# Kernel optimization log

Hardware: AMD Instinct MI355X
Metric: run time of the kernel (lower is better)

## Reference

```python
import jax, jax.numpy as jnp
import numpy as np

WS = (8, 8)          # window_size -> S = 64
NUM_HEADS = 4
DIM = 128


def _relative_position_index(ws):
    wh, ww = ws
    coords = np.stack(np.meshgrid(np.arange(wh), np.arange(ww), indexing='ij'))  # (2,Wh,Ww)
    cf = coords.reshape(2, -1)                                   # (2, Wh*Ww)
    rel = cf[:, :, None] - cf[:, None, :]                        # (2, S, S)
    rel = rel.transpose(1, 2, 0).astype(np.int64)                # (S, S, 2)
    rel[:, :, 0] += wh - 1
    rel[:, :, 1] += ww - 1
    rel[:, :, 0] *= 2 * ww - 1
    return rel.sum(-1)                                           # (S, S)


def setup_inputs() -> dict:
    key = jax.random.key(0)
    k = jax.random.split(key, 6)
    B, S, N, C = 128, WS[0] * WS[1], 32, DIM
    num_rel = (2 * WS[0] - 1) * (2 * WS[1] - 1)
    return {
        'x': jax.random.normal(k[0], (B, S, N, C), dtype=jnp.float32),
        'qkv_w': jax.random.normal(k[1], (3 * C, C), dtype=jnp.float32) * 0.02,
        'qkv_b': jnp.zeros((3 * C,), dtype=jnp.float32),
        'proj_w': jax.random.normal(k[2], (C, C), dtype=jnp.float32) * 0.02,
        'proj_b': jnp.zeros((C,), dtype=jnp.float32),
        'bias_table': jax.random.normal(k[3], (num_rel, NUM_HEADS), dtype=jnp.float32) * 0.02,
    }


def reference(x, qkv_w, qkv_b, proj_w, proj_b, bias_table):
    B, S, N, C = x.shape
    H = NUM_HEADS
    D = N * C // H                      # effective head dim
    scale = (C // H) ** -0.5            # matches head_dim = dim // num_heads in __init__

    xf = x.reshape(B, S * N, C)
    qkv = xf @ qkv_w.T + qkv_b          # (B, S*N, 3C)
    qkv = qkv.reshape(B, S, 3, H, D).transpose(2, 0, 3, 1, 4)  # (3, B, H, S, D)
    q, k, v = qkv[0], qkv[1], qkv[2]

    rel_idx = jnp.asarray(_relative_position_index(WS))        # (S, S) int
    bias = bias_table[rel_idx.reshape(-1)].reshape(S, S, H).transpose(2, 0, 1)  # (H,S,S)

    attn = jnp.einsum('bhsd,bhtd->bhst', q, k) * scale + bias[None]
    attn = jax.nn.softmax(attn, axis=-1)

    out = jnp.einsum('bhst,bhtd->bhsd', attn, v)               # (B,H,S,D)
    out = out.transpose(0, 2, 1, 3).reshape(B, S * N, C)
    out = out @ proj_w.T + proj_b
    return out.reshape(B, S, N, C)
```

## Files before the change

kernel.cpp:

```cpp
#include <hip/hip_runtime.h>
#include <cmath>


typedef short bf16x8 __attribute__((ext_vector_type(8)));
typedef float f32x4  __attribute__((ext_vector_type(4)));
#define MFMA16 __builtin_amdgcn_mfma_f32_16x16x32_bf16

__device__ __forceinline__ unsigned rne16(float f) {
    unsigned u = __float_as_uint(f);
    return (u + 0x7fffu + ((u >> 16) & 1u)) & 0xffff0000u;
}
__device__ __forceinline__ void cvt8(float4 a, float4 b, bf16x8& H, bf16x8& L) {
    float f[8] = {a.x, a.y, a.z, a.w, b.x, b.y, b.z, b.w};
    #pragma unroll
    for (int i = 0; i < 8; ++i) {
        unsigned r = rne16(f[i]);
        H[i] = (short)(r >> 16);
        float fh = __uint_as_float(r);
        L[i] = (short)(rne16(f[i] - fh) >> 16);
    }
}
__device__ __forceinline__ void cvt8h(float4 a, float4 b, bf16x8& H) {
    float f[8] = {a.x, a.y, a.z, a.w, b.x, b.y, b.z, b.w};
    #pragma unroll
    for (int i = 0; i < 8; ++i) H[i] = (short)(rne16(f[i]) >> 16);
}

__global__ void split_w(const float* __restrict__ qw, unsigned short* __restrict__ wsp) {
    int idx = blockIdx.x * 256 + threadIdx.x;
    if (idx >= 49152) return;
    int j = idx >> 7, c = idx & 127;
    float v = qw[idx];
    unsigned r = rne16(v);
    unsigned rl = rne16(v - __uint_as_float(r));
    int dest = (((j >> 5) * 16 + (c >> 3)) * 32 + (j & 31)) * 8 + (c & 7);
    wsp[dest] = (unsigned short)(r >> 16);
    wsp[49152 + dest] = (unsigned short)(rl >> 16);
}
__global__ void split_pw(const float* __restrict__ pw, unsigned short* __restrict__ pwsp) {
    int idx = blockIdx.x * 256 + threadIdx.x;
    if (idx >= 16384) return;
    int cp = idx >> 7, c = idx & 127;
    float v = pw[idx];
    unsigned r = rne16(v);
    unsigned rl = rne16(v - __uint_as_float(r));
    int dest = ((c >> 3) * 128 + cp) * 8 + (c & 7);
    pwsp[dest] = (unsigned short)(r >> 16);
    pwsp[16384 + dest] = (unsigned short)(rl >> 16);
}

constexpr int A9_QC0 = 0,     A9_KC0 = 8320;
constexpr int A9_QC1 = 16640, A9_KC1 = 24960;
constexpr int A9_P   = 33280;
constexpr int A9_SMA = 41600;
constexpr int A9_SMB = 42112;
constexpr int A9_VC0 = 0,     A9_VC1 = 8320;
constexpr int A9_LDS = 42624;

__global__ __launch_bounds__(512, 6)
void attn_mfma9(const float* __restrict__ x,
                const float* __restrict__ qkv_b,
                const float* __restrict__ bias_table,
                const unsigned short* __restrict__ wsp,
                float* __restrict__ out)
{
    __shared__ __attribute__((aligned(128))) char lds[A9_LDS];
    const int tid = threadIdx.x;
    const int lane = tid & 63;
    const int w = tid >> 6;
    const int l15 = lane & 15, lg = lane >> 4;
    const int qt = w & 3, ch = w >> 2;
    const int rowbase = qt * 16;
    const int b = blockIdx.x >> 2, h = blockIdx.x & 3;
    const float* __restrict__ xb = x + (size_t)b * 262144;
    const float* xrow0 = xb + (size_t)(rowbase + l15) * 4096 + lg * 8;

    bf16x8 aH[4];
    bf16x8 kH[4];
    int cur_na = -1, cur_nk = -1;

    auto loadfrags = [&](int n0, bf16x8 (&H)[4]) {
        const float* p = xrow0 + (size_t)n0 * 128;
        #pragma unroll
        for (int ks = 0; ks < 4; ++ks) {
            float4 a = *(const float4*)(p + ks * 32);
            float4 c = *(const float4*)(p + ks * 32 + 4);
            cvt8h(a, c, H[ks]);
        }
    };

    auto prod32 = [&](const bf16x8 (&H)[4], int j0, f32x4 (&acc)[2]) {
        const unsigned short* wb = wsp + (size_t)(j0 >> 5) * 4096;
        #pragma unroll
        for (int ks = 0; ks < 4; ++ks) {
            #pragma unroll
            for (int ct = 0; ct < 2; ++ct) {
                int gct = ch * 2 + ct;
                int ro = (gct >> 1) * 4096 + ((ks * 4 + lg) * 32 + (gct & 1) * 16 + l15) * 8;
                bf16x8 bh = *(const bf16x8*)(wb + ro);
                acc[ct] = MFMA16(H[ks], bh, acc[ct], 0, 0, 0);
            }
        }
    };

    auto storeP32 = [&](int base, f32x4 (&acc)[2], int j0) {
        #pragma unroll
        for (int ct = 0; ct < 2; ++ct) {
            int d = (ch * 2 + ct) * 16 + l15;
            float bias = qkv_b[j0 + d];
            int dofs = (d >> 3) * 1040 + (d & 7) * 2;
            #pragma unroll
            for (int reg = 0; reg < 4; ++reg) {
                int s = rowbase + lg * 4 + reg;
                *(unsigned short*)(lds + base + dofs + s * 16) =
                    (unsigned short)(rne16(acc[ct][reg] + bias) >> 16);
            }
        }
    };

    auto prodQK = [&](int cc) {
        int remq = h * 1024 + 64 * cc;
        int nq = remq / 384, j0q = remq - nq * 384;
        int remk = 4096 + h * 1024 + 64 * cc;
        int nk = remk / 384, j0k = remk - nk * 384;
        if (nq != cur_na) { loadfrags(nq, aH); cur_na = nq; }
        if (nk != cur_nk) { loadfrags(nk, kH); cur_nk = nk; }
        f32x4 qa[2];
        #pragma unroll
        for (int i = 0; i < 2; ++i) qa[i] = (f32x4){0.f, 0.f, 0.f, 0.f};
        prod32(aH, j0q, qa);
        storeP32((cc & 1) ? A9_QC1 : A9_QC0, qa, j0q);
        f32x4 ka[2];
        #pragma unroll
        for (int i = 0; i < 2; ++i) ka[i] = (f32x4){0.f, 0.f, 0.f, 0.f};
        prod32(kH, j0k, ka);
        storeP32((cc & 1) ? A9_KC1 : A9_KC0, ka, j0k);
    };

    f32x4 accQK[2];
    #pragma unroll
    for (int tt = 0; tt < 2; ++tt) accQK[tt] = (f32x4){0.f, 0.f, 0.f, 0.f};

    prodQK(0);
    __syncthreads();

    for (int cc = 0; cc < 16; ++cc) {
        if (cc < 15) prodQK(cc + 1);

        int qcb = (cc & 1) ? A9_QC1 : A9_QC0;
        int kcb = (cc & 1) ? A9_KC1 : A9_KC0;
        #pragma unroll
        for (int kst = 0; kst < 2; ++kst) {
            int grp = (kst * 4 + lg) * 1040;
            bf16x8 qh = *(const bf16x8*)(lds + qcb + grp + (rowbase + l15) * 16);
            #pragma unroll
            for (int tt = 0; tt < 2; ++tt) {
                int trow = ((ch * 2 + tt) * 16 + l15) * 16;
                bf16x8 kh = *(const bf16x8*)(lds + kcb + grp + trow);
                accQK[tt] = MFMA16(qh, kh, accQK[tt], 0, 0, 0);
            }
        }
        __syncthreads();
    }

    {
        const float scale = 0.17677669529663687f;
        float* smA = (float*)(lds + A9_SMA);
        float* smB = (float*)(lds + A9_SMB);
        float ex[4][2];
        #pragma unroll
        for (int reg = 0; reg < 4; ++reg) {
            int s = rowbase + lg * 4 + reg;
            int i1 = s >> 3, j1 = s & 7;
            float m = -1e30f;
            #pragma unroll
            for (int tt = 0; tt < 2; ++tt) {
                int t = (ch * 2 + tt) * 16 + l15;
                int i2 = t >> 3, j2 = t & 7;
                float L = accQK[tt][reg] * scale
                        + bias_table[((i1 - i2 + 7) * 15 + (j1 - j2 + 7)) * 4 + h];
                ex[reg][tt] = L;
                m = fmaxf(m, L);
            }
            m = fmaxf(m, __shfl_xor(m, 1));
            m = fmaxf(m, __shfl_xor(m, 2));
            m = fmaxf(m, __shfl_xor(m, 4));
            m = fmaxf(m, __shfl_xor(m, 8));
            if (l15 == 0) smA[ch * 64 + s] = m;
        }
        __syncthreads();
        #pragma unroll
        for (int reg = 0; reg < 4; ++reg) {
            int s = rowbase + lg * 4 + reg;
            float mg = fmaxf(smA[s], smA[64 + s]);
            float e0 = __expf(ex[reg][0] - mg);
            float e1 = __expf(ex[reg][1] - mg);
            ex[reg][0] = e0; ex[reg][1] = e1;
            float sum = e0 + e1;
            sum += __shfl_xor(sum, 1);
            sum += __shfl_xor(sum, 2);
            sum += __shfl_xor(sum, 4);
            sum += __shfl_xor(sum, 8);
            if (l15 == 0) smB[ch * 64 + s] = sum;
        }
        __syncthreads();
        #pragma unroll
        for (int reg = 0; reg < 4; ++reg) {
            int s = rowbase + lg * 4 + reg;
            float inv = 1.f / (smB[s] + smB[64 + s]);
            #pragma unroll
            for (int tt = 0; tt < 2; ++tt) {
                int t = (ch * 2 + tt) * 16 + l15;
                int off = (t >> 3) * 1040 + s * 16 + (t & 7) * 2;
                *(unsigned short*)(lds + A9_P + off) =
                    (unsigned short)(rne16(ex[reg][tt] * inv) >> 16);
            }
        }
    }

    cur_na = -1;
    float* ob = out + (size_t)b * 262144;

    auto prodV = [&](int cc) {
        int remv = 8192 + h * 1024 + 64 * cc;
        int nv = remv / 384, j0v = remv - nv * 384;
        if (nv != cur_na) { loadfrags(nv, aH); cur_na = nv; }
        f32x4 va[2];
        #pragma unroll
        for (int i = 0; i < 2; ++i) va[i] = (f32x4){0.f, 0.f, 0.f, 0.f};
        prod32(aH, j0v, va);
        int vcb = (cc & 1) ? A9_VC1 : A9_VC0;
        #pragma unroll
        for (int ct = 0; ct < 2; ++ct) {
            int d = (ch * 2 + ct) * 16 + l15;
            float bias = qkv_b[j0v + d];
            #pragma unroll
            for (int reg = 0; reg < 4; ++reg) {
                int t = rowbase + lg * 4 + reg;
                int off = (t >> 3) * 1040 + d * 16 + (t & 7) * 2;
                *(unsigned short*)(lds + vcb + off) =
                    (unsigned short)(rne16(va[ct][reg] + bias) >> 16);
            }
        }
    };

    prodV(0);
    __syncthreads();

    for (int cc = 0; cc < 16; ++cc) {
        if (cc < 15) prodV(cc + 1);

        int vcb = (cc & 1) ? A9_VC1 : A9_VC0;
        f32x4 o[2];
        #pragma unroll
        for (int i = 0; i < 2; ++i) o[i] = (f32x4){0.f, 0.f, 0.f, 0.f};
        #pragma unroll
        for (int kst = 0; kst < 2; ++kst) {
            bf16x8 pf = *(const bf16x8*)(lds + A9_P + (kst * 4 + lg) * 1040 + (rowbase + l15) * 16);
            int vgrp = (kst * 4 + lg) * 1040;
            #pragma unroll
            for (int dt = 0; dt < 2; ++dt) {
                int drow = ((ch * 2 + dt) * 16 + l15) * 16;
                bf16x8 vh = *(const bf16x8*)(lds + vcb + vgrp + drow);
                o[dt] = MFMA16(pf, vh, o[dt], 0, 0, 0);
            }
        }

        #pragma unroll
        for (int reg = 0; reg < 4; ++reg) {
            int s = rowbase + lg * 4 + reg;
            float* orow = ob + (size_t)(s * 32 + h * 8 + (cc >> 1)) * 128 + (cc & 1) * 64;
            #pragma unroll
            for (int dt = 0; dt < 2; ++dt)
                orow[(ch * 2 + dt) * 16 + l15] = o[dt][reg];
        }
        __syncthreads();
    }
}

__global__ __launch_bounds__(256, 4)
void proj_mfma(const unsigned short* __restrict__ pwsp,
               const float* __restrict__ pb,
               float* __restrict__ io)
{
    const int tid = threadIdx.x;
    const int lane = tid & 63;
    const int w = tid >> 6;
    const int l15 = lane & 15, lg = lane >> 4;
    const size_t rbase = (size_t)blockIdx.x * 64 + w * 16;

    const float* rp = io + (rbase + l15) * 128 + lg * 8;
    bf16x8 aH[4], aL[4];
    #pragma unroll
    for (int ks = 0; ks < 4; ++ks) {
        float4 a = *(const float4*)(rp + ks * 32);
        float4 c = *(const float4*)(rp + ks * 32 + 4);
        cvt8(a, c, aH[ks], aL[ks]);
    }

    f32x4 acc[8];
    #pragma unroll
    for (int i = 0; i < 8; ++i) acc[i] = (f32x4){0.f, 0.f, 0.f, 0.f};

    #pragma unroll
    for (int ks = 0; ks < 4; ++ks) {
        #pragma unroll
        for (int ct = 0; ct < 8; ++ct) {
            int ro = ((ks * 4 + lg) * 128 + ct * 16 + l15) * 8;
            bf16x8 bh = *(const bf16x8*)(pwsp + ro);
            bf16x8 bl = *(const bf16x8*)(pwsp + 16384 + ro);
            acc[ct] = MFMA16(aH[ks], bh, acc[ct], 0, 0, 0);
            acc[ct] = MFMA16(aH[ks], bl, acc[ct], 0, 0, 0);
            acc[ct] = MFMA16(aL[ks], bh, acc[ct], 0, 0, 0);
        }
    }

    #pragma unroll
    for (int ct = 0; ct < 8; ++ct) {
        float bias = pb[ct * 16 + l15];
        #pragma unroll
        for (int reg = 0; reg < 4; ++reg)
            io[(rbase + lg * 4 + reg) * 128 + ct * 16 + l15] = acc[ct][reg] + bias;
    }
}

constexpr int QC_OFF = 0;
constexpr int KC_OFF = 8320;
constexpr int VC_OFF = 24960;
constexpr int P_OFF  = 41856;
constexpr int LDS_TOT = 50176;

__global__ __launch_bounds__(256, 2)
void attn_mfma(const float* __restrict__ x,
               const float* __restrict__ qkv_b,
               const float* __restrict__ bias_table,
               const unsigned short* __restrict__ wsp,
               float* __restrict__ out)
{
    __shared__ __attribute__((aligned(128))) char lds[LDS_TOT];
    const int tid = threadIdx.x;
    const int lane = tid & 63;
    const int w = tid >> 6;
    const int l15 = lane & 15, lg = lane >> 4;
    const int rowbase = 16 * w;
    const int b = blockIdx.x >> 2, h = blockIdx.x & 3;
    const float* __restrict__ xb = x + (size_t)b * 262144;
    const float* xrow0 = xb + ((size_t)(rowbase + l15) * 32) * 128 + lg * 8;

    bf16x8 aH[4], aL[4];
    bf16x8 kH[4], kL[4];
    int cur_na = -1, cur_nk = -1;

    auto loadfrags = [&](int n0, bf16x8 (&H)[4], bf16x8 (&L)[4]) {
        const float* p = xrow0 + (size_t)n0 * 128;
        #pragma unroll
        for (int ks = 0; ks < 4; ++ks) {
            float4 a = *(const float4*)(p + ks * 32);
            float4 c = *(const float4*)(p + ks * 32 + 4);
            cvt8(a, c, H[ks], L[ks]);
        }
    };

    auto mm_band = [&](const bf16x8 (&H)[4], const bf16x8 (&L)[4], int band,
                       f32x4& a0, f32x4& a1) {
        const unsigned short* wb = wsp + (size_t)band * 4096;
        #pragma unroll
        for (int ks = 0; ks < 4; ++ks) {
            int ro = ((ks * 4 + lg) * 32 + l15) * 8;
            bf16x8 b0h = *(const bf16x8*)(wb + ro);
            bf16x8 b0l = *(const bf16x8*)(wb + 49152 + ro);
            bf16x8 b1h = *(const bf16x8*)(wb + ro + 128);
            bf16x8 b1l = *(const bf16x8*)(wb + 49152 + ro + 128);
            a0 = MFMA16(H[ks], b0h, a0, 0, 0, 0);
            a0 = MFMA16(H[ks], b0l, a0, 0, 0, 0);
            a0 = MFMA16(L[ks], b0h, a0, 0, 0, 0);
            a1 = MFMA16(H[ks], b1h, a1, 0, 0, 0);
            a1 = MFMA16(H[ks], b1l, a1, 0, 0, 0);
            a1 = MFMA16(L[ks], b1h, a1, 0, 0, 0);
        }
    };

    auto store_rc = [&](char* base, f32x4 a0, f32x4 a1, float b0, float b1) {
        #pragma unroll
        for (int reg = 0; reg < 4; ++reg) {
            int s = rowbase + lg * 4 + reg;
            {
                float v = a0[reg] + b0;
                int i = l15;
                int off = (i >> 3) * 1040 + s * 16 + (i & 7) * 2;
                unsigned r = rne16(v);
                *(unsigned short*)(base + off) = (unsigned short)(r >> 16);
                *(unsigned short*)(base + 4160 + off) =
                    (unsigned short)(rne16(v - __uint_as_float(r)) >> 16);
            }
            {
                float v = a1[reg] + b1;
                int i = 16 + l15;
                int off = (i >> 3) * 1040 + s * 16 + (i & 7) * 2;
                unsigned r = rne16(v);
                *(unsigned short*)(base + off) = (unsigned short)(r >> 16);
                *(unsigned short*)(base + 4160 + off) =
                    (unsigned short)(rne16(v - __uint_as_float(r)) >> 16);
            }
        }
    };

    f32x4 accQK[4];
    #pragma unroll
    for (int tt = 0; tt < 4; ++tt) accQK[tt] = (f32x4){0.f, 0.f, 0.f, 0.f};

    int buf = 0;
    for (int ccc = 0; ccc < 32; ++ccc) {
        int remq = h * 1024 + 32 * ccc;
        int nq = remq / 384, j0q = remq - nq * 384, bandq = j0q >> 5;
        int remk = 4096 + h * 1024 + 32 * ccc;
        int nk = remk / 384, j0k = remk - nk * 384, bandk = j0k >> 5;
        if (nq != cur_na) { loadfrags(nq, aH, aL); cur_na = nq; }
        if (nk != cur_nk) { loadfrags(nk, kH, kL); cur_nk = nk; }

        f32x4 q0 = (f32x4){0.f,0.f,0.f,0.f}, q1 = (f32x4){0.f,0.f,0.f,0.f};
        mm_band(aH, aL, bandq, q0, q1);
        store_rc(lds + QC_OFF, q0, q1, qkv_b[j0q + l15], qkv_b[j0q + 16 + l15]);

        f32x4 k0 = (f32x4){0.f,0.f,0.f,0.f}, k1 = (f32x4){0.f,0.f,0.f,0.f};
        mm_band(kH, kL, bandk, k0, k1);
        store_rc(lds + KC_OFF + buf * 8320, k0, k1, qkv_b[j0k + l15], qkv_b[j0k + 16 + l15]);

        __syncthreads();

        const char* qc = lds + QC_OFF + lg * 1040 + (rowbase + l15) * 16;
        bf16x8 qah = *(const bf16x8*)qc;
        bf16x8 qal = *(const bf16x8*)(qc + 4160);
        #pragma unroll
        for (int tt = 0; tt < 4; ++tt) {
            const char* kc = lds + KC_OFF + buf * 8320 + lg * 1040 + (tt * 16 + l15) * 16;
            bf16x8 kbh = *(const bf16x8*)kc;
            bf16x8 kbl = *(const bf16x8*)(kc + 4160);
            accQK[tt] = MFMA16(qah, kbh, accQK[tt], 0, 0, 0);
            accQK[tt] = MFMA16(qah, kbl, accQK[tt], 0, 0, 0);
            accQK[tt] = MFMA16(qal, kbh, accQK[tt], 0, 0, 0);
        }
        buf ^= 1;
    }

    {
        const float scale = 0.17677669529663687f;
        #pragma unroll
        for (int reg = 0; reg < 4; ++reg) {
            int s = rowbase + lg * 4 + reg;
            int i1 = s >> 3, j1 = s & 7;
            float Lv[4];
            float m = -1e30f;
            #pragma unroll
            for (int tt = 0; tt < 4; ++tt) {
                int t = tt * 16 + l15;
                int i2 = t >> 3, j2 = t & 7;
                float L = accQK[tt][reg] * scale
                        + bias_table[((i1 - i2 + 7) * 15 + (j1 - j2 + 7)) * 4 + h];
                Lv[tt] = L;
                m = fmaxf(m, L);
            }
            m = fmaxf(m, __shfl_xor(m, 1));
            m = fmaxf(m, __shfl_xor(m, 2));
            m = fmaxf(m, __shfl_xor(m, 4));
            m = fmaxf(m, __shfl_xor(m, 8));
            float sum = 0.f;
            #pragma unroll
            for (int tt = 0; tt < 4; ++tt) { Lv[tt] = __expf(Lv[tt] - m); sum += Lv[tt]; }
            sum += __shfl_xor(sum, 1);
            sum += __shfl_xor(sum, 2);
            sum += __shfl_xor(sum, 4);
            sum += __shfl_xor(sum, 8);
            float inv = 1.f / sum;
            #pragma unroll
            for (int tt = 0; tt < 4; ++tt) {
                int t = tt * 16 + l15;
                int off = (t >> 3) * 1040 + s * 16 + (t & 7) * 2;
                *(unsigned short*)(lds + P_OFF + off) = (unsigned short)(rne16(Lv[tt] * inv) >> 16);
            }
        }
    }

    cur_na = -1;
    int bufv = 0;
    float* ob = out + (size_t)b * 262144;
    for (int ccc = 0; ccc < 32; ++ccc) {
        int remv = 8192 + h * 1024 + 32 * ccc;
        int nv = remv / 384, j0v = remv - nv * 384, bandv = j0v >> 5;
        if (nv != cur_na) { loadfrags(nv, aH, aL); cur_na = nv; }

        f32x4 v0 = (f32x4){0.f,0.f,0.f,0.f}, v1 = (f32x4){0.f,0.f,0.f,0.f};
        mm_band(aH, aL, bandv, v0, v1);
        {
            char* base = lds + VC_OFF + bufv * 8448;
            float b0 = qkv_b[j0v + l15], b1 = qkv_b[j0v + 16 + l15];
            #pragma unroll
            for (int reg = 0; reg < 4; ++reg) {
                int t = rowbase + lg * 4 + reg;
                {
                    float v = v0[reg] + b0;
                    int i = l15;
                    int off = (t >> 3) * 528 + i * 16 + (t & 7) * 2;
                    unsigned r = rne16(v);
                    *(unsigned short*)(base + off) = (unsigned short)(r >> 16);
                    *(unsigned short*)(base + 4224 + off) =
                        (unsigned short)(rne16(v - __uint_as_float(r)) >> 16);
                }
                {
                    float v = v1[reg] + b1;
                    int i = 16 + l15;
                    int off = (t >> 3) * 528 + i * 16 + (t & 7) * 2;
                    unsigned r = rne16(v);
                    *(unsigned short*)(base + off) = (unsigned short)(r >> 16);
                    *(unsigned short*)(base + 4224 + off) =
                        (unsigned short)(rne16(v - __uint_as_float(r)) >> 16);
                }
            }
        }
        __syncthreads();

        f32x4 o0 = (f32x4){0.f,0.f,0.f,0.f}, o1 = (f32x4){0.f,0.f,0.f,0.f};
        #pragma unroll
        for (int ks = 0; ks < 2; ++ks) {
            bf16x8 pf = *(const bf16x8*)(lds + P_OFF + (ks * 4 + lg) * 1040 + (rowbase + l15) * 16);
            const char* vb = lds + VC_OFF + bufv * 8448 + (ks * 4 + lg) * 528;
            bf16x8 v0h = *(const bf16x8*)(vb + l15 * 16);
            bf16x8 v0l = *(const bf16x8*)(vb + 4224 + l15 * 16);
            bf16x8 v1h = *(const bf16x8*)(vb + (16 + l15) * 16);
            bf16x8 v1l = *(const bf16x8*)(vb + 4224 + (16 + l15) * 16);
            o0 = MFMA16(pf, v0h, o0, 0, 0, 0);
            o0 = MFMA16(pf, v0l, o0, 0, 0, 0);
            o1 = MFMA16(pf, v1h, o1, 0, 0, 0);
            o1 = MFMA16(pf, v1l, o1, 0, 0, 0);
        }
        bufv ^= 1;

        #pragma unroll
        for (int reg = 0; reg < 4; ++reg) {
            int s = rowbase + lg * 4 + reg;
            {
                int d = 32 * ccc + l15;
                ob[(s * 32 + h * 8 + (d >> 7)) * 128 + (d & 127)] = o0[reg];
            }
            {
                int d = 32 * ccc + 16 + l15;
                ob[(s * 32 + h * 8 + (d >> 7)) * 128 + (d & 127)] = o1[reg];
            }
        }
    }
}

constexpr int LDS_B = 128 * 132 + 64 * 132;

__global__ __launch_bounds__(256, 1)
void proj_inplace(const float* __restrict__ pw,
                  const float* __restrict__ pb,
                  float* __restrict__ io)
{
    __shared__ float lds[LDS_B];
    float* pwt  = lds;
    float* rows = lds + 128 * 132;
    const int tid = threadIdx.x;

    for (int idx = tid; idx < 128 * 128; idx += 256) {
        const int c = idx >> 7, cp = idx & 127;
        pwt[cp * 132 + c] = pw[idx];
    }
    const int rb = tid >> 5;
    const int cg = tid & 31;
    const float4 pbv = *(const float4*)(pb + cg * 4);

    for (int it = 0; it < 8; ++it) {
        const size_t base = ((size_t)blockIdx.x * 8 + it) * 64;
        __syncthreads();
        for (int f = tid; f < 64 * 32; f += 256) {
            const int r = f >> 5, c4 = f & 31;
            *(float4*)(rows + r * 132 + c4 * 4) =
                *(const float4*)(io + (base + r) * 128 + c4 * 4);
        }
        __syncthreads();
        float acc[8][4] = {};
        #pragma unroll 2
        for (int cp = 0; cp < 128; ++cp) {
            const float4 wv = *(const float4*)(pwt + cp * 132 + cg * 4);
            #pragma unroll
            for (int rr = 0; rr < 8; ++rr) {
                const float xv = rows[(rb * 8 + rr) * 132 + cp];
                acc[rr][0] += xv * wv.x;
                acc[rr][1] += xv * wv.y;
                acc[rr][2] += xv * wv.z;
                acc[rr][3] += xv * wv.w;
            }
        }
        #pragma unroll
        for (int rr = 0; rr < 8; ++rr) {
            float4 o;
            o.x = acc[rr][0] + pbv.x;
            o.y = acc[rr][1] + pbv.y;
            o.z = acc[rr][2] + pbv.z;
            o.w = acc[rr][3] + pbv.w;
            *(float4*)(io + (base + rb * 8 + rr) * 128 + cg * 4) = o;
        }
    }
}

extern "C" void kernel_launch(void* const* d_in, const int* in_sizes, int n_in,
                              void* d_out, int out_size, void* d_ws, size_t ws_size,
                              hipStream_t stream)
{
    const float* x          = (const float*)d_in[0];
    const float* qkv_w      = (const float*)d_in[1];
    const float* qkv_b      = (const float*)d_in[2];
    const float* proj_w     = (const float*)d_in[3];
    const float* proj_b     = (const float*)d_in[4];
    const float* bias_table = (const float*)d_in[5];
    float* out = (float*)d_out;

    if (ws_size >= 262144 && d_ws != nullptr) {
        unsigned short* wsp = (unsigned short*)d_ws;
        unsigned short* pwsp = wsp + 98304;
        split_w<<<dim3(192), dim3(256), 0, stream>>>(qkv_w, wsp);
        split_pw<<<dim3(64), dim3(256), 0, stream>>>(proj_w, pwsp);
        attn_mfma9<<<dim3(512), dim3(512), 0, stream>>>(x, qkv_b, bias_table, wsp, out);
        proj_mfma<<<dim3(4096), dim3(256), 0, stream>>>(pwsp, proj_b, out);
    } else if (ws_size >= 196608 && d_ws != nullptr) {
        unsigned short* wsp = (unsigned short*)d_ws;
        split_w<<<dim3(192), dim3(256), 0, stream>>>(qkv_w, wsp);
        attn_mfma<<<dim3(512), dim3(256), 0, stream>>>(x, qkv_b, bias_table, wsp, out);
        proj_inplace<<<dim3(512), dim3(256), 0, stream>>>(proj_w, proj_b, out);
    }
}
```

Before: 220.4 us.

## Split attention blocks by query half to double grid size

The fused attention kernel now launches 1024 blocks instead of 512, each handling 32 of the 64 query rows for one batch/head. Wave roles are remapped so Q projection, QK scores, softmax and PV each use one MFMA tile per wave, with smaller Q/P LDS buffers. This raises parallelism and lowers LDS use per block. In exchange, each block still computes the full K and V projections, so that work is duplicated across the two query halves and total reads of x and FLOPs rise.

```diff
diff --git a/kernel.cpp b/kernel.cpp
--- a/kernel.cpp
+++ b/kernel.cpp
@@ -49,70 +49,114 @@
     pwsp[16384 + dest] = (unsigned short)(rl >> 16);
 }
 
-constexpr int A9_QC0 = 0,     A9_KC0 = 8320;
-constexpr int A9_QC1 = 16640, A9_KC1 = 24960;
-constexpr int A9_P   = 33280;
-constexpr int A9_SMA = 41600;
-constexpr int A9_SMB = 42112;
-constexpr int A9_VC0 = 0,     A9_VC1 = 8320;
-constexpr int A9_LDS = 42624;
+constexpr int A12_QC0 = 0,     A12_KC0 = 4224;
+constexpr int A12_QC1 = 12544, A12_KC1 = 16768;
+constexpr int A12_P   = 25088;
+constexpr int A12_SMA = 29312;
+constexpr int A12_SMB = 29824;
+constexpr int A12_VC0 = 0,     A12_VC1 = 12544;
+constexpr int A12_LDS = 30336;
 
 __global__ __launch_bounds__(512, 6)
-void attn_mfma9(const float* __restrict__ x,
-                const float* __restrict__ qkv_b,
-                const float* __restrict__ bias_table,
-                const unsigned short* __restrict__ wsp,
-                float* __restrict__ out)
+void attn_mfma12(const float* __restrict__ x,
+                 const float* __restrict__ qkv_b,
+                 const float* __restrict__ bias_table,
+                 const unsigned short* __restrict__ wsp,
+                 float* __restrict__ out)
 {
-    __shared__ __attribute__((aligned(128))) char lds[A9_LDS];
+    __shared__ __attribute__((aligned(128))) char lds[A12_LDS];
     const int tid = threadIdx.x;
     const int lane = tid & 63;
     const int w = tid >> 6;
     const int l15 = lane & 15, lg = lane >> 4;
-    const int qt = w & 3, ch = w >> 2;
-    const int rowbase = qt * 16;
-    const int b = blockIdx.x >> 2, h = blockIdx.x & 3;
+    const int b = blockIdx.x >> 3;
+    const int h = (blockIdx.x >> 1) & 3;
+    const int sh = blockIdx.x & 1;
+    const int s_base = sh * 32;
+
+    const int qrt = w & 1, qcq = w >> 1;
+    const int krt = w & 3, kch = w >> 2;
+    const int cqt = w & 1, ctt = w >> 1;
+    const int pqt = w & 1, pch = w >> 1;
+
     const float* __restrict__ xb = x + (size_t)b * 262144;
-    const float* xrow0 = xb + (size_t)(rowbase + l15) * 4096 + lg * 8;
-
-    bf16x8 aH[4];
-    bf16x8 kH[4];
-    int cur_na = -1, cur_nk = -1;
-
-    auto loadfrags = [&](int n0, bf16x8 (&H)[4]) {
-        const float* p = xrow0 + (size_t)n0 * 128;
+    const float* xq = xb + (size_t)(s_base + qrt * 16 + l15) * 4096 + lg * 8;
+    const float* xk = xb + (size_t)(krt * 16 + l15) * 4096 + lg * 8;
+
+    bf16x8 qF[4], kF[4];
+    int cur_nq = -1, cur_nk = -1;
+
+    auto loadQ = [&](int n0) {
+        const float* p = xq + (size_t)n0 * 128;
+        #pragma unroll
+        for (int ks = 0; ks < 4; ++ks)
+            cvt8h(*(const float4*)(p + ks * 32), *(const float4*)(p + ks * 32 + 4), qF[ks]);
+    };
+    auto loadK = [&](int n0) {
+        const float* p = xk + (size_t)n0 * 128;
+        #pragma unroll
+        for (int ks = 0; ks < 4; ++ks)
+            cvt8h(*(const float4*)(p + ks * 32), *(const float4*)(p + ks * 32 + 4), kF[ks]);
+    };
+
+    auto prodQ = [&](int j0, f32x4& acc) {
+        const unsigned short* wb = wsp + (size_t)((j0 >> 5) + (qcq >> 1)) * 4096;
+        const int co = ((qcq & 1) * 16 + l15) * 8;
         #pragma unroll
         for (int ks = 0; ks < 4; ++ks) {
-            float4 a = *(const float4*)(p + ks * 32);
-            float4 c = *(const float4*)(p + ks * 32 + 4);
-            cvt8h(a, c, H[ks]);
-        }
-    };
-
-    auto prod32 = [&](const bf16x8 (&H)[4], int j0, f32x4 (&acc)[2]) {
-        const unsigned short* wb = wsp + (size_t)(j0 >> 5) * 4096;
-        #pragma unroll
-        for (int ks = 0; ks < 4; ++ks) {
-            #pragma unroll
-            for (int ct = 0; ct < 2; ++ct) {
-                int gct = ch * 2 + ct;
-                int ro = (gct >> 1) * 4096 + ((ks * 4 + lg) * 32 + (gct & 1) * 16 + l15) * 8;
-                bf16x8 bh = *(const bf16x8*)(wb + ro);
-                acc[ct] = MFMA16(H[ks], bh, acc[ct], 0, 0, 0);
-            }
-        }
-    };
-
-    auto storeP32 = [&](int base, f32x4 (&acc)[2], int j0) {
+            bf16x8 bh = *(const bf16x8*)(wb + (ks * 4 + lg) * 256 + co);
+            acc = MFMA16(qF[ks], bh, acc, 0, 0, 0);
+        }
+    };
+    auto prodKV = [&](int j0, f32x4 (&acc)[2]) {
         #pragma unroll
         for (int ct = 0; ct < 2; ++ct) {
-            int d = (ch * 2 + ct) * 16 + l15;
-            float bias = qkv_b[j0 + d];
-            int dofs = (d >> 3) * 1040 + (d & 7) * 2;
+            int gct = kch * 2 + ct;
+            const unsigned short* wb = wsp + (size_t)((j0 >> 5) + (gct >> 1)) * 4096;
+            const int co = ((gct & 1) * 16 + l15) * 8;
+            #pragma unroll
+            for (int ks = 0; ks < 4; ++ks) {
+                bf16x8 bh = *(const bf16x8*)(wb + (ks * 4 + lg) * 256 + co);
+                acc[ct] = MFMA16(kF[ks], bh, acc[ct], 0, 0, 0);
+            }
+        }
+    };
+
+    auto storeQ = [&](int base, f32x4& acc, int j0) {
+        int c = qcq * 16 + l15;
+        float bias = qkv_b[j0 + c];
+        int cofs = (c >> 3) * 528 + (c & 7) * 2;
+        #pragma unroll
+        for (int reg = 0; reg < 4; ++reg) {
+            int sl = qrt * 16 + lg * 4 + reg;
+            *(unsigned short*)(lds + base + cofs + sl * 16) =
+                (unsigned short)(rne16(acc[reg] + bias) >> 16);
+        }
+    };
+    auto storeK = [&](int base, f32x4 (&acc)[2], int j0) {
+        #pragma unroll
+        for (int ct = 0; ct < 2; ++ct) {
+            int c = kch * 32 + ct * 16 + l15;
+            float bias = qkv_b[j0 + c];
+            int cofs = (c >> 3) * 1040 + (c & 7) * 2;
             #pragma unroll
             for (int reg = 0; reg < 4; ++reg) {
-                int s = rowbase + lg * 4 + reg;
-                *(unsigned short*)(lds + base + dofs + s * 16) =
+                int t = krt * 16 + lg * 4 + reg;
+                *(unsigned short*)(lds + base + cofs + t * 16) =
+                    (unsigned short)(rne16(acc[ct][reg] + bias) >> 16);
+            }
+        }
+    };
+    auto storeV = [&](int base, f32x4 (&acc)[2], int j0) {
+        #pragma unroll
+        for (int ct = 0; ct < 2; ++ct) {
+            int c = kch * 32 + ct * 16 + l15;
+            float bias = qkv_b[j0 + c];
+            #pragma unroll
+            for (int reg = 0; reg < 4; ++reg) {
+                int t = krt * 16 + lg * 4 + reg;
+                int off = (t >> 3) * 1040 + c * 16 + (t & 7) * 2;
+                *(unsigned short*)(lds + base + off) =
                     (unsigned short)(rne16(acc[ct][reg] + bias) >> 16);
             }
         }
@@ -123,23 +167,19 @@
         int nq = remq / 384, j0q = remq - nq * 384;
         int remk = 4096 + h * 1024 + 64 * cc;
         int nk = remk / 384, j0k = remk - nk * 384;
-        if (nq != cur_na) { loadfrags(nq, aH); cur_na = nq; }
-        if (nk != cur_nk) { loadfrags(nk, kH); cur_nk = nk; }
-        f32x4 qa[2];
-        #pragma unroll
-        for (int i = 0; i < 2; ++i) qa[i] = (f32x4){0.f, 0.f, 0.f, 0.f};
-        prod32(aH, j0q, qa);
-        storeP32((cc & 1) ? A9_QC1 : A9_QC0, qa, j0q);
+        if (nq != cur_nq) { loadQ(nq); cur_nq = nq; }
+        if (nk != cur_nk) { loadK(nk); cur_nk = nk; }
+        f32x4 qa = (f32x4){0.f, 0.f, 0.f, 0.f};
+        prodQ(j0q, qa);
+        storeQ((cc & 1) ? A12_QC1 : A12_QC0, qa, j0q);
         f32x4 ka[2];
-        #pragma unroll
-        for (int i = 0; i < 2; ++i) ka[i] = (f32x4){0.f, 0.f, 0.f, 0.f};
-        prod32(kH, j0k, ka);
-        storeP32((cc & 1) ? A9_KC1 : A9_KC0, ka, j0k);
-    };
-
-    f32x4 accQK[2];
-    #pragma unroll
-    for (int tt = 0; tt < 2; ++tt) accQK[tt] = (f32x4){0.f, 0.f, 0.f, 0.f};
+        ka[0] = (f32x4){0.f, 0.f, 0.f, 0.f};
+        ka[1] = (f32x4){0.f, 0.f, 0.f, 0.f};
+        prodKV(j0k, ka);
+        storeK((cc & 1) ? A12_KC1 : A12_KC0, ka, j0k);
+    };
+
+    f32x4 accQK = (f32x4){0.f, 0.f, 0.f, 0.f};
 
     prodQK(0);
     __syncthreads();
@@ -147,101 +187,78 @@
     for (int cc = 0; cc < 16; ++cc) {
         if (cc < 15) prodQK(cc + 1);
 
-        int qcb = (cc & 1) ? A9_QC1 : A9_QC0;
-        int kcb = (cc & 1) ? A9_KC1 : A9_KC0;
+        int qcb = (cc & 1) ? A12_QC1 : A12_QC0;
+        int kcb = (cc & 1) ? A12_KC1 : A12_KC0;
         #pragma unroll
         for (int kst = 0; kst < 2; ++kst) {
-            int grp = (kst * 4 + lg) * 1040;
-            bf16x8 qh = *(const bf16x8*)(lds + qcb + grp + (rowbase + l15) * 16);
-            #pragma unroll
-            for (int tt = 0; tt < 2; ++tt) {
-                int trow = ((ch * 2 + tt) * 16 + l15) * 16;
-                bf16x8 kh = *(const bf16x8*)(lds + kcb + grp + trow);
-                accQK[tt] = MFMA16(qh, kh, accQK[tt], 0, 0, 0);
-            }
+            int grp = kst * 4 + lg;
+            bf16x8 qh = *(const bf16x8*)(lds + qcb + grp * 528 + (cqt * 16 + l15) * 16);
+            bf16x8 kh = *(const bf16x8*)(lds + kcb + grp * 1040 + (ctt * 16 + l15) * 16);
+            accQK = MFMA16(qh, kh, accQK, 0, 0, 0);
         }
         __syncthreads();
     }
 
     {
         const float scale = 0.17677669529663687f;
-        float* smA = (float*)(lds + A9_SMA);
-        float* smB = (float*)(lds + A9_SMB);
-        float ex[4][2];
-        #pragma unroll
-        for (int reg = 0; reg < 4; ++reg) {
-            int s = rowbase + lg * 4 + reg;
-            int i1 = s >> 3, j1 = s & 7;
-            float m = -1e30f;
-            #pragma unroll
-            for (int tt = 0; tt < 2; ++tt) {
-                int t = (ch * 2 + tt) * 16 + l15;
-                int i2 = t >> 3, j2 = t & 7;
-                float L = accQK[tt][reg] * scale
-                        + bias_table[((i1 - i2 + 7) * 15 + (j1 - j2 + 7)) * 4 + h];
-                ex[reg][tt] = L;
-                m = fmaxf(m, L);
-            }
+        float* smA = (float*)(lds + A12_SMA);
+        float* smB = (float*)(lds + A12_SMB);
+        float ex[4];
+        #pragma unroll
+        for (int reg = 0; reg < 4; ++reg) {
+            int sl = cqt * 16 + lg * 4 + reg;
+            int sg = s_base + sl;
+            int i1 = sg >> 3, j1 = sg & 7;
+            int t = ctt * 16 + l15;
+            int i2 = t >> 3, j2 = t & 7;
+            float L = accQK[reg] * scale
+                    + bias_table[((i1 - i2 + 7) * 15 + (j1 - j2 + 7)) * 4 + h];
+            ex[reg] = L;
+            float m = L;
             m = fmaxf(m, __shfl_xor(m, 1));
             m = fmaxf(m, __shfl_xor(m, 2));
             m = fmaxf(m, __shfl_xor(m, 4));
             m = fmaxf(m, __shfl_xor(m, 8));
-            if (l15 == 0) smA[ch * 64 + s] = m;
-        }
-        __syncthreads();
-        #pragma unroll
-        for (int reg = 0; reg < 4; ++reg) {
-            int s = rowbase + lg * 4 + reg;
-            float mg = fmaxf(smA[s], smA[64 + s]);
-            float e0 = __expf(ex[reg][0] - mg);
-            float e1 = __expf(ex[reg][1] - mg);
-            ex[reg][0] = e0; ex[reg][1] = e1;
-            float sum = e0 + e1;
+            if (l15 == 0) smA[ctt * 32 + sl] = m;
+        }
+        __syncthreads();
+        #pragma unroll
+        for (int reg = 0; reg < 4; ++reg) {
+            int sl = cqt * 16 + lg * 4 + reg;
+            float mg = fmaxf(fmaxf(smA[sl], smA[32 + sl]), fmaxf(smA[64 + sl], smA[96 + sl]));
+            float e = __expf(ex[reg] - mg);
+            ex[reg] = e;
+            float sum = e;
             sum += __shfl_xor(sum, 1);
             sum += __shfl_xor(sum, 2);
             sum += __shfl_xor(sum, 4);
             sum += __shfl_xor(sum, 8);
-            if (l15 == 0) smB[ch * 64 + s] = sum;
-        }
-        __syncthreads();
-        #pragma unroll
-        for (int reg = 0; reg < 4; ++reg) {
-            int s = rowbase + lg * 4 + reg;
-            float inv = 1.f / (smB[s] + smB[64 + s]);
-            #pragma unroll
-            for (int tt = 0; tt < 2; ++tt) {
-                int t = (ch * 2 + tt) * 16 + l15;
-                int off = (t >> 3) * 1040 + s * 16 + (t & 7) * 2;
-                *(unsigned short*)(lds + A9_P + off) =
-                    (unsigned short)(rne16(ex[reg][tt] * inv) >> 16);
-            }
-        }
-    }
-
-    cur_na = -1;
+            if (l15 == 0) smB[ctt * 32 + sl] = sum;
+        }
+        __syncthreads();
+        #pragma unroll
+        for (int reg = 0; reg < 4; ++reg) {
+            int sl = cqt * 16 + lg * 4 + reg;
+            float inv = 1.f / (smB[sl] + smB[32 + sl] + smB[64 + sl] + smB[96 + sl]);
+            int t = ctt * 16 + l15;
+            int off = (t >> 3) * 528 + sl * 16 + (t & 7) * 2;
+            *(unsigned short*)(lds + A12_P + off) =
+                (unsigned short)(rne16(ex[reg] * inv) >> 16);
+        }
+    }
+
+    cur_nk = -1;
     float* ob = out + (size_t)b * 262144;
 
     auto prodV = [&](int cc) {
         int remv = 8192 + h * 1024 + 64 * cc;
         int nv = remv / 384, j0v = remv - nv * 384;
-        if (nv != cur_na) { loadfrags(nv, aH); cur_na = nv; }
+        if (nv != cur_nk) { loadK(nv); cur_nk = nv; }
         f32x4 va[2];
-        #pragma unroll
-        for (int i = 0; i < 2; ++i) va[i] = (f32x4){0.f, 0.f, 0.f, 0.f};
-        prod32(aH, j0v, va);
-        int vcb = (cc & 1) ? A9_VC1 : A9_VC0;
-        #pragma unroll
-        for (int ct = 0; ct < 2; ++ct) {
-            int d = (ch * 2 + ct) * 16 + l15;
-            float bias = qkv_b[j0v + d];
-            #pragma unroll
-            for (int reg = 0; reg < 4; ++reg) {
-                int t = rowbase + lg * 4 + reg;
-                int off = (t >> 3) * 1040 + d * 16 + (t & 7) * 2;
-                *(unsigned short*)(lds + vcb + off) =
-                    (unsigned short)(rne16(va[ct][reg] + bias) >> 16);
-            }
-        }
+        va[0] = (f32x4){0.f, 0.f, 0.f, 0.f};
+        va[1] = (f32x4){0.f, 0.f, 0.f, 0.f};
+        prodKV(j0v, va);
+        storeV((cc & 1) ? A12_VC1 : A12_VC0, va, j0v);
     };
 
     prodV(0);
@@ -250,29 +267,21 @@
     for (int cc = 0; cc < 16; ++cc) {
         if (cc < 15) prodV(cc + 1);
 
-        int vcb = (cc & 1) ? A9_VC1 : A9_VC0;
-        f32x4 o[2];
-        #pragma unroll
-        for (int i = 0; i < 2; ++i) o[i] = (f32x4){0.f, 0.f, 0.f, 0.f};
+        int vcb = (cc & 1) ? A12_VC1 : A12_VC0;
+        f32x4 o = (f32x4){0.f, 0.f, 0.f, 0.f};
         #pragma unroll
         for (int kst = 0; kst < 2; ++kst) {
-            bf16x8 pf = *(const bf16x8*)(lds + A9_P + (kst * 4 + lg) * 1040 + (rowbase + l15) * 16);
-            int vgrp = (kst * 4 + lg) * 1040;
-            #pragma unroll
-            for (int dt = 0; dt < 2; ++dt) {
-                int drow = ((ch * 2 + dt) * 16 + l15) * 16;
-                bf16x8 vh = *(const bf16x8*)(lds + vcb + vgrp + drow);
-                o[dt] = MFMA16(pf, vh, o[dt], 0, 0, 0);
-            }
-        }
-
-        #pragma unroll
-        for (int reg = 0; reg < 4; ++reg) {
-            int s = rowbase + lg * 4 + reg;
-            float* orow = ob + (size_t)(s * 32 + h * 8 + (cc >> 1)) * 128 + (cc & 1) * 64;
-            #pragma unroll
-            for (int dt = 0; dt < 2; ++dt)
-                orow[(ch * 2 + dt) * 16 + l15] = o[dt][reg];
+            int grp = kst * 4 + lg;
+            bf16x8 pf = *(const bf16x8*)(lds + A12_P + grp * 528 + (pqt * 16 + l15) * 16);
+            bf16x8 vh = *(const bf16x8*)(lds + vcb + grp * 1040 + (pch * 16 + l15) * 16);
+            o = MFMA16(pf, vh, o, 0, 0, 0);
+        }
+
+        #pragma unroll
+        for (int reg = 0; reg < 4; ++reg) {
+            int sg = s_base + pqt * 16 + lg * 4 + reg;
+            float* orow = ob + (size_t)(sg * 32 + h * 8 + (cc >> 1)) * 128 + (cc & 1) * 64;
+            orow[pch * 16 + l15] = o[reg];
         }
         __syncthreads();
     }
@@ -621,7 +630,7 @@
         unsigned short* pwsp = wsp + 98304;
         split_w<<<dim3(192), dim3(256), 0, stream>>>(qkv_w, wsp);
         split_pw<<<dim3(64), dim3(256), 0, stream>>>(proj_w, pwsp);
-        attn_mfma9<<<dim3(512), dim3(512), 0, stream>>>(x, qkv_b, bias_table, wsp, out);
+        attn_mfma12<<<dim3(1024), dim3(512), 0, stream>>>(x, qkv_b, bias_table, wsp, out);
         proj_mfma<<<dim3(4096), dim3(256), 0, stream>>>(pwsp, proj_b, out);
     } else if (ws_size >= 196608 && d_ws != nullptr) {
         unsigned short* wsp = (unsigned short*)d_ws;
```

Measured after the change: 290.5 us. 31.8% more time.

## Widen attention block to 16 waves with 128-column chunks

Applied to the files above, without the earlier changes.

The attention kernel now uses 1024 threads per block (16 waves) instead of 512, splitting column work four ways instead of two and processing 128-wide chunks in 8 iterations instead of 64-wide chunks in 16. This halves the number of barrier-separated iterations and spreads the QK, softmax and PV work over more waves to raise parallelism per block. The cost is double the LDS per block (about 77KB), which limits resident blocks per CU, plus larger per-barrier synchronization among 16 waves. Softmax reductions now combine four partial maxima and sums through shared memory.

```diff
diff --git a/kernel.cpp b/kernel.cpp
--- a/kernel.cpp
+++ b/kernel.cpp
@@ -49,27 +49,27 @@
     pwsp[16384 + dest] = (unsigned short)(rl >> 16);
 }
 
-constexpr int A9_QC0 = 0,     A9_KC0 = 8320;
-constexpr int A9_QC1 = 16640, A9_KC1 = 24960;
-constexpr int A9_P   = 33280;
-constexpr int A9_SMA = 41600;
-constexpr int A9_SMB = 42112;
-constexpr int A9_VC0 = 0,     A9_VC1 = 8320;
-constexpr int A9_LDS = 42624;
-
-__global__ __launch_bounds__(512, 6)
-void attn_mfma9(const float* __restrict__ x,
-                const float* __restrict__ qkv_b,
-                const float* __restrict__ bias_table,
-                const unsigned short* __restrict__ wsp,
-                float* __restrict__ out)
+constexpr int A16_QC0 = 0,     A16_KC0 = 16640;
+constexpr int A16_QC1 = 33280, A16_KC1 = 49920;
+constexpr int A16_P   = 66560;
+constexpr int A16_SMA = 74880;
+constexpr int A16_SMB = 75904;
+constexpr int A16_VC0 = 0,     A16_VC1 = 16640;
+constexpr int A16_LDS = 76928;
+
+__global__ __launch_bounds__(1024, 8)
+void attn_mfma16(const float* __restrict__ x,
+                 const float* __restrict__ qkv_b,
+                 const float* __restrict__ bias_table,
+                 const unsigned short* __restrict__ wsp,
+                 float* __restrict__ out)
 {
-    __shared__ __attribute__((aligned(128))) char lds[A9_LDS];
+    __shared__ __attribute__((aligned(128))) char lds[A16_LDS];
     const int tid = threadIdx.x;
     const int lane = tid & 63;
     const int w = tid >> 6;
     const int l15 = lane & 15, lg = lane >> 4;
-    const int qt = w & 3, ch = w >> 2;
+    const int qt = w & 3, cq = w >> 2;
     const int rowbase = qt * 16;
     const int b = blockIdx.x >> 2, h = blockIdx.x & 3;
     const float* __restrict__ xb = x + (size_t)b * 262144;
@@ -90,23 +90,21 @@
     };
 
     auto prod32 = [&](const bf16x8 (&H)[4], int j0, f32x4 (&acc)[2]) {
-        const unsigned short* wb = wsp + (size_t)(j0 >> 5) * 4096;
+        const unsigned short* wb = wsp + (size_t)(j0 >> 5) * 4096 + (size_t)cq * 4096;
         #pragma unroll
         for (int ks = 0; ks < 4; ++ks) {
-            #pragma unroll
-            for (int ct = 0; ct < 2; ++ct) {
-                int gct = ch * 2 + ct;
-                int ro = (gct >> 1) * 4096 + ((ks * 4 + lg) * 32 + (gct & 1) * 16 + l15) * 8;
-                bf16x8 bh = *(const bf16x8*)(wb + ro);
-                acc[ct] = MFMA16(H[ks], bh, acc[ct], 0, 0, 0);
-            }
+            const int rb_ = ((ks * 4 + lg) * 32 + l15) * 8;
+            bf16x8 b0 = *(const bf16x8*)(wb + rb_);
+            bf16x8 b1 = *(const bf16x8*)(wb + rb_ + 128);
+            acc[0] = MFMA16(H[ks], b0, acc[0], 0, 0, 0);
+            acc[1] = MFMA16(H[ks], b1, acc[1], 0, 0, 0);
         }
     };
 
     auto storeP32 = [&](int base, f32x4 (&acc)[2], int j0) {
         #pragma unroll
         for (int ct = 0; ct < 2; ++ct) {
-            int d = (ch * 2 + ct) * 16 + l15;
+            int d = (cq * 2 + ct) * 16 + l15;
             float bias = qkv_b[j0 + d];
             int dofs = (d >> 3) * 1040 + (d & 7) * 2;
             #pragma unroll
@@ -119,102 +117,88 @@
     };
 
     auto prodQK = [&](int cc) {
-        int remq = h * 1024 + 64 * cc;
+        int remq = h * 1024 + 128 * cc;
         int nq = remq / 384, j0q = remq - nq * 384;
-        int remk = 4096 + h * 1024 + 64 * cc;
+        int remk = 4096 + h * 1024 + 128 * cc;
         int nk = remk / 384, j0k = remk - nk * 384;
         if (nq != cur_na) { loadfrags(nq, aH); cur_na = nq; }
         if (nk != cur_nk) { loadfrags(nk, kH); cur_nk = nk; }
         f32x4 qa[2];
-        #pragma unroll
-        for (int i = 0; i < 2; ++i) qa[i] = (f32x4){0.f, 0.f, 0.f, 0.f};
+        qa[0] = (f32x4){0.f, 0.f, 0.f, 0.f};
+        qa[1] = (f32x4){0.f, 0.f, 0.f, 0.f};
         prod32(aH, j0q, qa);
-        storeP32((cc & 1) ? A9_QC1 : A9_QC0, qa, j0q);
+        storeP32((cc & 1) ? A16_QC1 : A16_QC0, qa, j0q);
         f32x4 ka[2];
-        #pragma unroll
-        for (int i = 0; i < 2; ++i) ka[i] = (f32x4){0.f, 0.f, 0.f, 0.f};
+        ka[0] = (f32x4){0.f, 0.f, 0.f, 0.f};
+        ka[1] = (f32x4){0.f, 0.f, 0.f, 0.f};
         prod32(kH, j0k, ka);
-        storeP32((cc & 1) ? A9_KC1 : A9_KC0, ka, j0k);
-    };
-
-    f32x4 accQK[2];
-    #pragma unroll
-    for (int tt = 0; tt < 2; ++tt) accQK[tt] = (f32x4){0.f, 0.f, 0.f, 0.f};
+        storeP32((cc & 1) ? A16_KC1 : A16_KC0, ka, j0k);
+    };
+
+    f32x4 accQK = (f32x4){0.f, 0.f, 0.f, 0.f};
 
     prodQK(0);
     __syncthreads();
 
-    for (int cc = 0; cc < 16; ++cc) {
-        if (cc < 15) prodQK(cc + 1);
-
-        int qcb = (cc & 1) ? A9_QC1 : A9_QC0;
-        int kcb = (cc & 1) ? A9_KC1 : A9_KC0;
-        #pragma unroll
-        for (int kst = 0; kst < 2; ++kst) {
+    for (int cc = 0; cc < 8; ++cc) {
+        if (cc < 7) prodQK(cc + 1);
+
+        int qcb = (cc & 1) ? A16_QC1 : A16_QC0;
+        int kcb = (cc & 1) ? A16_KC1 : A16_KC0;
+        #pragma unroll
+        for (int kst = 0; kst < 4; ++kst) {
             int grp = (kst * 4 + lg) * 1040;
             bf16x8 qh = *(const bf16x8*)(lds + qcb + grp + (rowbase + l15) * 16);
-            #pragma unroll
-            for (int tt = 0; tt < 2; ++tt) {
-                int trow = ((ch * 2 + tt) * 16 + l15) * 16;
-                bf16x8 kh = *(const bf16x8*)(lds + kcb + grp + trow);
-                accQK[tt] = MFMA16(qh, kh, accQK[tt], 0, 0, 0);
-            }
+            bf16x8 kh = *(const bf16x8*)(lds + kcb + grp + (cq * 16 + l15) * 16);
+            accQK = MFMA16(qh, kh, accQK, 0, 0, 0);
         }
         __syncthreads();
     }
 
     {
         const float scale = 0.17677669529663687f;
-        float* smA = (float*)(lds + A9_SMA);
-        float* smB = (float*)(lds + A9_SMB);
-        float ex[4][2];
+        float* smA = (float*)(lds + A16_SMA);
+        float* smB = (float*)(lds + A16_SMB);
+        float ex[4];
         #pragma unroll
         for (int reg = 0; reg < 4; ++reg) {
             int s = rowbase + lg * 4 + reg;
             int i1 = s >> 3, j1 = s & 7;
-            float m = -1e30f;
-            #pragma unroll
-            for (int tt = 0; tt < 2; ++tt) {
-                int t = (ch * 2 + tt) * 16 + l15;
-                int i2 = t >> 3, j2 = t & 7;
-                float L = accQK[tt][reg] * scale
-                        + bias_table[((i1 - i2 + 7) * 15 + (j1 - j2 + 7)) * 4 + h];
-                ex[reg][tt] = L;
-                m = fmaxf(m, L);
-            }
+            int t = cq * 16 + l15;
+            int i2 = t >> 3, j2 = t & 7;
+            float L = accQK[reg] * scale
+                    + bias_table[((i1 - i2 + 7) * 15 + (j1 - j2 + 7)) * 4 + h];
+            ex[reg] = L;
+            float m = L;
             m = fmaxf(m, __shfl_xor(m, 1));
             m = fmaxf(m, __shfl_xor(m, 2));
             m = fmaxf(m, __shfl_xor(m, 4));
             m = fmaxf(m, __shfl_xor(m, 8));
-            if (l15 == 0) smA[ch * 64 + s] = m;
+            if (l15 == 0) smA[cq * 64 + s] = m;
         }
         __syncthreads();
         #pragma unroll
         for (int reg = 0; reg < 4; ++reg) {
             int s = rowbase + lg * 4 + reg;
-            float mg = fmaxf(smA[s], smA[64 + s]);
-            float e0 = __expf(ex[reg][0] - mg);
-            float e1 = __expf(ex[reg][1] - mg);
-            ex[reg][0] = e0; ex[reg][1] = e1;
-            float sum = e0 + e1;
+            float mg = fmaxf(fmaxf(smA[s], smA[64 + s]), fmaxf(smA[128 + s], smA[192 + s]));
+            float e = __expf(ex[reg] - mg);
+            ex[reg] = e;
+            float sum = e;
             sum += __shfl_xor(sum, 1);
             sum += __shfl_xor(sum, 2);
             sum += __shfl_xor(sum, 4);
             sum += __shfl_xor(sum, 8);
-            if (l15 == 0) smB[ch * 64 + s] = sum;
+            if (l15 == 0) smB[cq * 64 + s] = sum;
         }
         __syncthreads();
         #pragma unroll
         for (int reg = 0; reg < 4; ++reg) {
             int s = rowbase + lg * 4 + reg;
-            float inv = 1.f / (smB[s] + smB[64 + s]);
-            #pragma unroll
-            for (int tt = 0; tt < 2; ++tt) {
-                int t = (ch * 2 + tt) * 16 + l15;
-                int off = (t >> 3) * 1040 + s * 16 + (t & 7) * 2;
-                *(unsigned short*)(lds + A9_P + off) =
-                    (unsigned short)(rne16(ex[reg][tt] * inv) >> 16);
-            }
+            float inv = 1.f / (smB[s] + smB[64 + s] + smB[128 + s] + smB[192 + s]);
+            int t = cq * 16 + l15;
+            int off = (t >> 3) * 1040 + s * 16 + (t & 7) * 2;
+            *(unsigned short*)(lds + A16_P + off) =
+                (unsigned short)(rne16(ex[reg] * inv) >> 16);
         }
     }
 
@@ -222,22 +206,22 @@
     float* ob = out + (size_t)b * 262144;
 
     auto prodV = [&](int cc) {
-        int remv = 8192 + h * 1024 + 64 * cc;
+        int remv = 8192 + h * 1024 + 128 * cc;
         int nv = remv / 384, j0v = remv - nv * 384;
         if (nv != cur_na) { loadfrags(nv, aH); cur_na = nv; }
         f32x4 va[2];
-        #pragma unroll
-        for (int i = 0; i < 2; ++i) va[i] = (f32x4){0.f, 0.f, 0.f, 0.f};
+        va[0] = (f32x4){0.f, 0.f, 0.f, 0.f};
+        va[1] = (f32x4){0.f, 0.f, 0.f, 0.f};
         prod32(aH, j0v, va);
-        int vcb = (cc & 1) ? A9_VC1 : A9_VC0;
+        int vcb = (cc & 1) ? A16_VC1 : A16_VC0;
         #pragma unroll
         for (int ct = 0; ct < 2; ++ct) {
-            int d = (ch * 2 + ct) * 16 + l15;
+            int d = (cq * 2 + ct) * 16 + l15;
             float bias = qkv_b[j0v + d];
             #pragma unroll
             for (int reg = 0; reg < 4; ++reg) {
                 int t = rowbase + lg * 4 + reg;
-                int off = (t >> 3) * 1040 + d * 16 + (t & 7) * 2;
+                int off = (t >> 3) * 2080 + d * 16 + (t & 7) * 2;
                 *(unsigned short*)(lds + vcb + off) =
                     (unsigned short)(rne16(va[ct][reg] + bias) >> 16);
             }
@@ -247,20 +231,20 @@
     prodV(0);
     __syncthreads();
 
-    for (int cc = 0; cc < 16; ++cc) {
-        if (cc < 15) prodV(cc + 1);
-
-        int vcb = (cc & 1) ? A9_VC1 : A9_VC0;
+    for (int cc = 0; cc < 8; ++cc) {
+        if (cc < 7) prodV(cc + 1);
+
+        int vcb = (cc & 1) ? A16_VC1 : A16_VC0;
         f32x4 o[2];
-        #pragma unroll
-        for (int i = 0; i < 2; ++i) o[i] = (f32x4){0.f, 0.f, 0.f, 0.f};
+        o[0] = (f32x4){0.f, 0.f, 0.f, 0.f};
+        o[1] = (f32x4){0.f, 0.f, 0.f, 0.f};
         #pragma unroll
         for (int kst = 0; kst < 2; ++kst) {
-            bf16x8 pf = *(const bf16x8*)(lds + A9_P + (kst * 4 + lg) * 1040 + (rowbase + l15) * 16);
-            int vgrp = (kst * 4 + lg) * 1040;
+            bf16x8 pf = *(const bf16x8*)(lds + A16_P + (kst * 4 + lg) * 1040 + (rowbase + l15) * 16);
+            int vgrp = (kst * 4 + lg) * 2080;
             #pragma unroll
             for (int dt = 0; dt < 2; ++dt) {
-                int drow = ((ch * 2 + dt) * 16 + l15) * 16;
+                int drow = ((cq * 2 + dt) * 16 + l15) * 16;
                 bf16x8 vh = *(const bf16x8*)(lds + vcb + vgrp + drow);
                 o[dt] = MFMA16(pf, vh, o[dt], 0, 0, 0);
             }
@@ -269,10 +253,10 @@
         #pragma unroll
         for (int reg = 0; reg < 4; ++reg) {
             int s = rowbase + lg * 4 + reg;
-            float* orow = ob + (size_t)(s * 32 + h * 8 + (cc >> 1)) * 128 + (cc & 1) * 64;
+            float* orow = ob + (size_t)(s * 32 + h * 8 + cc) * 128;
             #pragma unroll
             for (int dt = 0; dt < 2; ++dt)
-                orow[(ch * 2 + dt) * 16 + l15] = o[dt][reg];
+                orow[(cq * 2 + dt) * 16 + l15] = o[dt][reg];
         }
         __syncthreads();
     }
@@ -621,7 +605,7 @@
         unsigned short* pwsp = wsp + 98304;
         split_w<<<dim3(192), dim3(256), 0, stream>>>(qkv_w, wsp);
         split_pw<<<dim3(64), dim3(256), 0, stream>>>(proj_w, pwsp);
-        attn_mfma9<<<dim3(512), dim3(512), 0, stream>>>(x, qkv_b, bias_table, wsp, out);
+        attn_mfma16<<<dim3(512), dim3(1024), 0, stream>>>(x, qkv_b, bias_table, wsp, out);
         proj_mfma<<<dim3(4096), dim3(256), 0, stream>>>(pwsp, proj_b, out);
     } else if (ws_size >= 196608 && d_ws != nullptr) {
         unsigned short* wsp = (unsigned short*)d_ws;
```

Result: slower. 319.2 us (+44.8%).
